# Kernel optimization log

Measured on AMD Instinct MI355X. Metric: run time of the kernel, lower is better.

Reference implementation:

```python
import jax, jax.numpy as jnp
import numpy as np

B, T, C = 4, 2048, 1024
NH = 16
HS = C // NH


def setup_inputs() -> dict:
    key = jax.random.key(0)
    k1, k2, k3, k4, k5 = jax.random.split(key, 5)
    scale = 1.0 / np.sqrt(C)
    return {
        "x": jax.random.normal(k1, (B, T, C), dtype=jnp.float32),
        "Wk": jax.random.normal(k2, (C, C), dtype=jnp.float32) * scale,
        "Wq": jax.random.normal(k3, (C, C), dtype=jnp.float32) * scale,
        "Wv": jax.random.normal(k4, (C, C), dtype=jnp.float32) * scale,
        "Wp": jax.random.normal(k5, (C, C), dtype=jnp.float32) * scale,
    }


def reference(x, Wk, Wq, Wv, Wp):
    b, t, c = x.shape
    # projections (nn.Linear with bias=False computes x @ W.T; weights here are
    # stored so that x @ W is equivalent -- same math, random init either way)
    k = (x @ Wk).reshape(b, t, NH, HS).transpose(0, 2, 1, 3)  # [B,H,T,hs]
    q = (x @ Wq).reshape(b, t, NH, HS).transpose(0, 2, 1, 3)
    v = (x @ Wv).reshape(b, t, NH, HS).transpose(0, 2, 1, 3)
    att = jnp.einsum("bhqd,bhkd->bhqk", q, k) / jnp.sqrt(jnp.float32(HS))
    causal = jnp.tril(jnp.ones((t, t), dtype=bool))
    att = jnp.where(causal[None, None, :, :], att, -jnp.inf)
    att = jax.nn.softmax(att, axis=-1)
    y = jnp.einsum("bhqk,bhkd->bhqd", att, v)  # [B,H,T,hs]
    y = y.transpose(0, 2, 1, 3).reshape(b, t, c)
    return y @ Wp
```

## Files before the change

### kernel.cpp

```cpp
#include <hip/hip_runtime.h>
#include <cstddef>
#include <cstdint>


namespace {

typedef unsigned short u16;
typedef unsigned int u32;
typedef __attribute__((ext_vector_type(8))) short s8v;
typedef __attribute__((ext_vector_type(4))) short s4v;
typedef __attribute__((ext_vector_type(4))) float f4v;

constexpr int Bn = 4, Tn = 2048, Cn = 1024;
constexpr int Mn = Bn * Tn;
constexpr int KVB = 128;
constexpr int NT128 = Tn / 128;
constexpr float QSCALE = 0.125f * 1.44269504f;

__device__ __forceinline__ u16 bfc(float f) {
  return __builtin_bit_cast(u16, (__bf16)f);
}

__device__ __forceinline__ float ex2(float x) {
#if __has_builtin(__builtin_amdgcn_exp2f)
  return __builtin_amdgcn_exp2f(x);
#else
  return exp2f(x);
#endif
}

__device__ __forceinline__ f4v mfma16(s8v a, s8v b, f4v c) {
  return __builtin_amdgcn_mfma_f32_16x16x32_bf16(a, b, c, 0, 0, 0);
}

__device__ __forceinline__ f4v mfma16k16(s4v a, s4v b, f4v c) {
#if __has_builtin(__builtin_amdgcn_mfma_f32_16x16x16bf16_1k)
  return __builtin_amdgcn_mfma_f32_16x16x16bf16_1k(a, b, c, 0, 0, 0);
#else
  f4v d = c;
  asm("v_mfma_f32_16x16x16_bf16 %0, %1, %2, %0" : "+v"(d) : "v"(a), "v"(b));
  return d;
#endif
}

typedef __attribute__((address_space(1))) const u32 gas_u32;
typedef __attribute__((address_space(3))) u32 las_u32;
__device__ __forceinline__ void gl_lds16(const void* g, void* l) {
  __builtin_amdgcn_global_load_lds((gas_u32*)g, (las_u32*)l, 16, 0, 0);
}

__global__ __launch_bounds__(256) void cvtx(const float* __restrict__ in,
                                            u16* __restrict__ out) {
  const size_t i = ((size_t)blockIdx.x * 256 + threadIdx.x) * 8;
  const float4 a = *(const float4*)(in + i);
  const float4 b = *(const float4*)(in + i + 4);
  alignas(16) u16 t[8] = {bfc(a.x), bfc(a.y), bfc(a.z), bfc(a.w),
                          bfc(b.x), bfc(b.y), bfc(b.z), bfc(b.w)};
  *(s8v*)(out + i) = *(const s8v*)t;
}

__global__ __launch_bounds__(256) void wtrans(
    const float* __restrict__ w0, const float* __restrict__ w1,
    const float* __restrict__ w2, const float* __restrict__ w3,
    u16* __restrict__ o0, u16* __restrict__ o1, u16* __restrict__ o2,
    u16* __restrict__ o3) {
  const float* W;
  u16* O;
  switch (blockIdx.z) {
    case 0: W = w0; O = o0; break;
    case 1: W = w1; O = o1; break;
    case 2: W = w2; O = o2; break;
    default: W = w3; O = o3; break;
  }
  __shared__ float Tsh[64][65];
  const int tid = threadIdx.x;
  const int n0 = blockIdx.x * 64, k0 = blockIdx.y * 64;
  {
    const int rk = tid >> 2, c0 = (tid & 3) * 16;
#pragma unroll
    for (int u = 0; u < 4; ++u) {
      const float4 v = *(const float4*)&W[(size_t)(k0 + rk) * Cn + n0 + c0 + u * 4];
      Tsh[rk][c0 + u * 4 + 0] = v.x;
      Tsh[rk][c0 + u * 4 + 1] = v.y;
      Tsh[rk][c0 + u * 4 + 2] = v.z;
      Tsh[rk][c0 + u * 4 + 3] = v.w;
    }
  }
  __syncthreads();
  {
    const int rn = tid >> 2, ck0 = (tid & 3) * 16;
    alignas(16) u16 t[16];
#pragma unroll
    for (int u = 0; u < 16; ++u) t[u] = bfc(Tsh[ck0 + u][rn]);
    *(s8v*)&O[(size_t)(n0 + rn) * Cn + k0 + ck0] = *(const s8v*)&t[0];
    *(s8v*)&O[(size_t)(n0 + rn) * Cn + k0 + ck0 + 8] = *(const s8v*)&t[8];
  }
}

template <int OUT_MODE>
__device__ __forceinline__ void gemm_body(const u16* __restrict__ A,
                                          const u16* __restrict__ Bt,
                                          void* __restrict__ Cout, int bm,
                                          int bn, u16* As, u16* Bs) {
  const int N = Cn, K = Cn;
  const int tid = threadIdx.x;
  const int l = tid & 63, w = tid >> 6;
  const int lr = l & 15, lh = l >> 4;
  const int lrow = tid >> 2;
  const int lkcol = (tid & 3) * 8;
  const u16* Ag = A + (size_t)(bm * 128 + lrow) * K + lkcol;
  const u16* Bg = Bt + (size_t)(bn * 128 + lrow) * K + lkcol;
  const int wm = (w >> 1) * 64, wn = (w & 1) * 64;
  f4v acc[4][4] = {};
  for (int k0 = 0; k0 < K; k0 += 32) {
    __syncthreads();
    gl_lds16(Ag + k0, &As[(size_t)tid * 8]);
    gl_lds16(Ag + (size_t)64 * K + k0, &As[2048 + (size_t)tid * 8]);
    gl_lds16(Bg + k0, &Bs[(size_t)tid * 8]);
    gl_lds16(Bg + (size_t)64 * K + k0, &Bs[2048 + (size_t)tid * 8]);
    __syncthreads();
    s8v af[4], bfr[4];
#pragma unroll
    for (int i = 0; i < 4; ++i)
      af[i] = *(const s8v*)&As[(wm + i * 16 + lr) * 32 + lh * 8];
#pragma unroll
    for (int j = 0; j < 4; ++j)
      bfr[j] = *(const s8v*)&Bs[(wn + j * 16 + lr) * 32 + lh * 8];
    __builtin_amdgcn_s_setprio(1);
#pragma unroll
    for (int i = 0; i < 4; ++i)
#pragma unroll
      for (int j = 0; j < 4; ++j)
        acc[i][j] = mfma16(af[i], bfr[j], acc[i][j]);
    __builtin_amdgcn_s_setprio(0);
  }
  if (OUT_MODE == 2) {
    float* Cf = (float*)Cout;
#pragma unroll
    for (int i = 0; i < 4; ++i) {
      const int row = bm * 128 + wm + i * 16 + lh * 4;
#pragma unroll
      for (int j = 0; j < 4; ++j) {
        const int col = bn * 128 + wn + j * 16 + lr;
#pragma unroll
        for (int r = 0; r < 4; ++r)
          Cf[(size_t)(row + r) * N + col] = acc[i][j][r];
      }
    }
  } else if (OUT_MODE == 0 || OUT_MODE == 3) {
    u16* Cb = (u16*)Cout;
    const float sc = (OUT_MODE == 3) ? QSCALE : 1.0f;
#pragma unroll
    for (int i = 0; i < 4; ++i) {
      const int row = bm * 128 + wm + i * 16 + lh * 4;
#pragma unroll
      for (int j = 0; j < 4; ++j) {
        const int col = bn * 128 + wn + j * 16 + lr;
#pragma unroll
        for (int r = 0; r < 4; ++r)
          Cb[(size_t)(row + r) * N + col] = bfc(acc[i][j][r] * sc);
      }
    }
  } else {
    u16* Vt = (u16*)Cout;
#pragma unroll
    for (int i = 0; i < 4; ++i) {
      const int row0 = bm * 128 + wm + i * 16 + lh * 4;
      const int bq = row0 >> 11;
      const int t0g = row0 & 2047;
      const int tau = t0g & 127;
      const int taup = ((tau >> 5) << 5) | (((tau >> 2) & 3) << 3) |
                       (((tau >> 4) & 1) << 2);
      const int t0p = (t0g & ~127) | taup;
#pragma unroll
      for (int j = 0; j < 4; ++j) {
        const int col = bn * 128 + wn + j * 16 + lr;
        const int hh = col >> 6, dd = col & 63;
        alignas(8) u16 t4[4];
#pragma unroll
        for (int r = 0; r < 4; ++r) t4[r] = bfc(acc[i][j][r]);
        *(s4v*)&Vt[((size_t)((bq * 16 + hh) * 64 + dd)) * Tn + t0p] =
            *(const s4v*)t4;
      }
    }
  }
}

__global__ __launch_bounds__(256) void gemm_qkv(
    const u16* __restrict__ A, const u16* __restrict__ btq,
    const u16* __restrict__ btk, const u16* __restrict__ btv,
    u16* __restrict__ qb, u16* __restrict__ kb, u16* __restrict__ vt) {
  __shared__ __align__(16) u16 As[4096], Bs[4096];
  const int bid = blockIdx.x;
  const int wg = (bid & 7) * 192 + (bid >> 3);
  const int which = wg >> 9, inner = wg & 511;
  const int bm = inner & 63, bn = inner >> 6;
  if (which == 0)
    gemm_body<3>(A, btq, qb, bm, bn, As, Bs);
  else if (which == 1)
    gemm_body<0>(A, btk, kb, bm, bn, As, Bs);
  else
    gemm_body<1>(A, btv, vt, bm, bn, As, Bs);
}

template <int OUT_MODE>
__global__ __launch_bounds__(256) void gemm_bt(const u16* __restrict__ A,
                                               const u16* __restrict__ Bt,
                                               void* __restrict__ Cout) {
  __shared__ __align__(16) u16 As[4096], Bs[4096];
  const int bid = blockIdx.x;
  const int wg = (bid & 7) * 64 + (bid >> 3);
  const int bm = wg & 63, bn = wg >> 6;
  gemm_body<OUT_MODE>(A, Bt, Cout, bm, bn, As, Bs);
}

__device__ __forceinline__ void stage_kv(const u16* __restrict__ kgb,
                                         const u16* __restrict__ vtb,
                                         u16* __restrict__ Kb,
                                         u16* __restrict__ Vb, int k0,
                                         int tid) {
#pragma unroll
  for (int is = 0; is < 2; ++is) {
    const int slot = is * 512 + tid;
    const int row = slot >> 3, ch = slot & 7;
    gl_lds16(kgb + (size_t)(k0 + row) * Cn + ((ch ^ (row & 7)) * 8),
             &Kb[slot * 8]);
  }
#pragma unroll
  for (int is = 0; is < 2; ++is) {
    const int slot = is * 512 + tid;
    const int d = slot >> 4, ch = slot & 15;
    gl_lds16(vtb + (size_t)d * Tn + k0 + ((ch ^ (d & 7)) * 8), &Vb[slot * 8]);
  }
}

__device__ __forceinline__ void attn_step(const s8v (&aq)[2],
                                          const u16* __restrict__ Ks,
                                          const u16* __restrict__ Vs, int kb0,
                                          int kb1, const int (&vch)[4], int ln,
                                          int lh, bool diag, int k0, int qg,
                                          float& m_i, float& l_i, f4v* o) {
  f4v s[8] = {};
  __builtin_amdgcn_s_setprio(1);
#pragma unroll
  for (int n = 0; n < 8; ++n) {
    const s8v bk0 = *(const s8v*)&Ks[kb0 + n * 1024];
    const s8v bk1 = *(const s8v*)&Ks[kb1 + n * 1024];
    s[n] = mfma16(bk0, aq[0], s[n]);
    s[n] = mfma16(bk1, aq[1], s[n]);
  }
  __builtin_amdgcn_s_setprio(0);
  float rm = -1e30f;
  if (diag) {
#pragma unroll
    for (int n = 0; n < 8; ++n)
#pragma unroll
      for (int r = 0; r < 4; ++r) {
        float x = s[n][r];
        if (k0 + n * 16 + lh * 4 + r > qg) x = -1e30f;
        s[n][r] = x;
        rm = fmaxf(rm, x);
      }
  } else {
#pragma unroll
    for (int n = 0; n < 8; ++n)
      rm = fmaxf(rm, fmaxf(fmaxf(s[n][0], s[n][1]), fmaxf(s[n][2], s[n][3])));
  }
  if (!__all(rm <= m_i + 11.5f)) {
    float rr = fmaxf(rm, __shfl_xor(rm, 16));
    rr = fmaxf(rr, __shfl_xor(rr, 32));
    const float mnew = fmaxf(m_i, rr);
    const float al = ex2(m_i - mnew);
    m_i = mnew;
    l_i *= al;
#pragma unroll
    for (int r = 0; r < 4; ++r) {
      const float ar = __shfl(al, (ln & 48) | (lh * 4 + r));
#pragma unroll
      for (int n2 = 0; n2 < 4; ++n2) o[n2][r] *= ar;
    }
  }
  s4v pa[8];
  float rs = 0.f;
#pragma unroll
  for (int n = 0; n < 8; ++n) {
    const float p0 = ex2(s[n][0] - m_i);
    const float p1 = ex2(s[n][1] - m_i);
    const float p2 = ex2(s[n][2] - m_i);
    const float p3 = ex2(s[n][3] - m_i);
    rs += (p0 + p1) + (p2 + p3);
    pa[n] = (s4v){(short)bfc(p0), (short)bfc(p1), (short)bfc(p2),
                  (short)bfc(p3)};
  }
  l_i += rs;
  __builtin_amdgcn_s_setprio(1);
#pragma unroll
  for (int n2 = 0; n2 < 4; ++n2) {
#pragma unroll
    for (int p = 0; p < 4; ++p) {
      const s8v vv = *(const s8v*)&Vs[vch[p] + n2 * 2048];
      const s4v lo = {vv[0], vv[1], vv[2], vv[3]};
      const s4v hi = {vv[4], vv[5], vv[6], vv[7]};
      o[n2] = mfma16k16(pa[2 * p], lo, o[n2]);
      o[n2] = mfma16k16(pa[2 * p + 1], hi, o[n2]);
    }
  }
  __builtin_amdgcn_s_setprio(0);
}

__global__ __launch_bounds__(512) void attn_big(const u16* __restrict__ qg,
                                                const u16* __restrict__ kg,
                                                const u16* __restrict__ vtg,
                                                u16* __restrict__ yg) {
  __shared__ __align__(16) u16 Ks0[KVB * 64], Ks1[KVB * 64];
  __shared__ __align__(16) u16 Vs0[64 * KVB], Vs1[64 * KVB];
  const int tid = threadIdx.x;
  const int ln = tid & 63, w = tid >> 6;
  const int lr = ln & 15, lh = ln >> 4;
  const int bid = blockIdx.x;
  const int wg = (bid & 7) * 64 + (bid >> 3);
  const int bh = wg >> 3, xp = wg & 7;
  const int b = bh >> 4, h = bh & 15;
  const int tL = xp, tH = NT128 - 1 - xp;
  const int q0L = tL * 128, q0H = tH * 128;
  const u16* kgb = kg + (size_t)(b * Tn) * Cn + h * 64;
  const u16* vtb = vtg + (size_t)(bh * 64) * Tn;
  const int kb0 = lr * 64 + ((lh) ^ (lr & 7)) * 8;
  const int kb1 = lr * 64 + ((4 + lh) ^ (lr & 7)) * 8;
  int vch[4];
#pragma unroll
  for (int p = 0; p < 4; ++p)
    vch[p] = lr * 128 + ((p * 4 + lh) ^ (lr & 7)) * 8;
  s8v aqL[2], aqH[2];
  {
    const int row = w * 16 + lr;
#pragma unroll
    for (int kd = 0; kd < 2; ++kd) {
      aqL[kd] = *(const s8v*)&qg[(size_t)(b * Tn + q0L + row) * Cn + h * 64 +
                                 kd * 32 + lh * 8];
      aqH[kd] = *(const s8v*)&qg[(size_t)(b * Tn + q0H + row) * Cn + h * 64 +
                                 kd * 32 + lh * 8];
    }
  }
  const int qgH = q0H + w * 16 + lr;
  const int qgL = q0L + w * 16 + lr;
  float mL = -1e30f, lL = 0.f, mH = -1e30f, lH = 0.f;
  f4v oL[4] = {}, oH[4] = {};
  stage_kv(kgb, vtb, Ks0, Vs0, 0, tid);
  __syncthreads();
  for (int kt = 0; kt <= tH; ++kt) {
    const bool cur = kt & 1;
    const u16* Kb = cur ? Ks1 : Ks0;
    const u16* Vb = cur ? Vs1 : Vs0;
    if (kt < tH)
      stage_kv(kgb, vtb, cur ? Ks0 : Ks1, cur ? Vs0 : Vs1, (kt + 1) * KVB,
               tid);
    attn_step(aqH, Kb, Vb, kb0, kb1, vch, ln, lh, kt == tH, kt * KVB, qgH, mH,
              lH, oH);
    if (kt <= tL)
      attn_step(aqL, Kb, Vb, kb0, kb1, vch, ln, lh, kt == tL, kt * KVB, qgL,
                mL, lL, oL);
    __syncthreads();
  }
  {
    float ls = lH;
    ls += __shfl_xor(ls, 16);
    ls += __shfl_xor(ls, 32);
    const float linv = 1.0f / ls;
#pragma unroll
    for (int r = 0; r < 4; ++r) {
      const float iv = __shfl(linv, (ln & 48) | (lh * 4 + r));
      const int row = q0H + w * 16 + lh * 4 + r;
#pragma unroll
      for (int n2 = 0; n2 < 4; ++n2)
        yg[(size_t)(b * Tn + row) * Cn + h * 64 + n2 * 16 + lr] =
            bfc(oH[n2][r] * iv);
    }
  }
  {
    float ls = lL;
    ls += __shfl_xor(ls, 16);
    ls += __shfl_xor(ls, 32);
    const float linv = 1.0f / ls;
#pragma unroll
    for (int r = 0; r < 4; ++r) {
      const float iv = __shfl(linv, (ln & 48) | (lh * 4 + r));
      const int row = q0L + w * 16 + lh * 4 + r;
#pragma unroll
      for (int n2 = 0; n2 < 4; ++n2)
        yg[(size_t)(b * Tn + row) * Cn + h * 64 + n2 * 16 + lr] =
            bfc(oL[n2][r] * iv);
    }
  }
}

}

extern "C" void kernel_launch(void* const* d_in, const int* in_sizes, int n_in,
                              void* d_out, int out_size, void* d_ws,
                              size_t ws_size, hipStream_t stream) {
  (void)in_sizes; (void)n_in; (void)out_size; (void)ws_size;
  const float* x = (const float*)d_in[0];
  const float* Wk = (const float*)d_in[1];
  const float* Wq = (const float*)d_in[2];
  const float* Wv = (const float*)d_in[3];
  const float* Wp = (const float*)d_in[4];
  float* out = (float*)d_out;
  char* ws = (char*)d_ws;

  u16* xb = (u16*)(ws);
  u16* wqt = (u16*)(ws + 16777216);
  u16* wkt = (u16*)(ws + 18874368);
  u16* wvt = (u16*)(ws + 20971520);
  u16* wpt = (u16*)(ws + 23068672);
  u16* qb = (u16*)(ws + 25165824);
  u16* kb = (u16*)(ws + 41943040);
  u16* vt = (u16*)(ws + 58720256);
  u16* yb = (u16*)(ws + 75497472);

  cvtx<<<dim3(4096), dim3(256), 0, stream>>>(x, xb);
  wtrans<<<dim3(16, 16, 4), dim3(256), 0, stream>>>(Wq, Wk, Wv, Wp, wqt, wkt,
                                                    wvt, wpt);
  gemm_qkv<<<dim3(1536), dim3(256), 0, stream>>>(xb, wqt, wkt, wvt, qb, kb,
                                                 vt);
  attn_big<<<dim3(512), dim3(512), 0, stream>>>(qb, kb, vt, yb);
  gemm_bt<2><<<dim3(512), dim3(256), 0, stream>>>(yb, wpt, out);
}
```

Measured before the change: 186.6 us.

## Merge prep kernels, deepen GEMM K-tile with XOR-swizzled LDS, remap blocks per XCD

Folds the x-to-bf16 conversion and the weight transpose into a single prep launch, removing one kernel launch. The GEMM K step grows from 32 to 64, which halves the barrier pairs per tile at the cost of double the LDS per block. An XOR swizzle on the LDS columns is meant to avoid bank conflicts on the 128-byte rows. Block-to-tile mapping is changed so each XCD handles a contiguous band of M rows, aiming for better L2 reuse of A.

```diff
diff --git a/kernel.cpp b/kernel.cpp
--- a/kernel.cpp
+++ b/kernel.cpp
@@ -49,32 +49,35 @@
   __builtin_amdgcn_global_load_lds((gas_u32*)g, (las_u32*)l, 16, 0, 0);
 }
 
-__global__ __launch_bounds__(256) void cvtx(const float* __restrict__ in,
-                                            u16* __restrict__ out) {
-  const size_t i = ((size_t)blockIdx.x * 256 + threadIdx.x) * 8;
-  const float4 a = *(const float4*)(in + i);
-  const float4 b = *(const float4*)(in + i + 4);
-  alignas(16) u16 t[8] = {bfc(a.x), bfc(a.y), bfc(a.z), bfc(a.w),
-                          bfc(b.x), bfc(b.y), bfc(b.z), bfc(b.w)};
-  *(s8v*)(out + i) = *(const s8v*)t;
-}
-
-__global__ __launch_bounds__(256) void wtrans(
+__global__ __launch_bounds__(256) void prep(
+    const float* __restrict__ x, u16* __restrict__ xb,
     const float* __restrict__ w0, const float* __restrict__ w1,
     const float* __restrict__ w2, const float* __restrict__ w3,
     u16* __restrict__ o0, u16* __restrict__ o1, u16* __restrict__ o2,
     u16* __restrict__ o3) {
+  __shared__ float Tsh[64][65];
+  const int bid = blockIdx.x;
+  const int tid = threadIdx.x;
+  if (bid < 4096) {
+    const size_t i = ((size_t)bid * 256 + tid) * 8;
+    const float4 a = *(const float4*)(x + i);
+    const float4 b = *(const float4*)(x + i + 4);
+    alignas(16) u16 t[8] = {bfc(a.x), bfc(a.y), bfc(a.z), bfc(a.w),
+                            bfc(b.x), bfc(b.y), bfc(b.z), bfc(b.w)};
+    *(s8v*)(xb + i) = *(const s8v*)t;
+    return;
+  }
+  const int idx = bid - 4096;
+  const int wz = idx >> 8, wy = (idx >> 4) & 15, wx = idx & 15;
   const float* W;
   u16* O;
-  switch (blockIdx.z) {
+  switch (wz) {
     case 0: W = w0; O = o0; break;
     case 1: W = w1; O = o1; break;
     case 2: W = w2; O = o2; break;
     default: W = w3; O = o3; break;
   }
-  __shared__ float Tsh[64][65];
-  const int tid = threadIdx.x;
-  const int n0 = blockIdx.x * 64, k0 = blockIdx.y * 64;
+  const int n0 = wx * 64, k0 = wy * 64;
   {
     const int rk = tid >> 2, c0 = (tid & 3) * 16;
 #pragma unroll
@@ -106,33 +109,45 @@
   const int tid = threadIdx.x;
   const int l = tid & 63, w = tid >> 6;
   const int lr = l & 15, lh = l >> 4;
-  const int lrow = tid >> 2;
-  const int lkcol = (tid & 3) * 8;
-  const u16* Ag = A + (size_t)(bm * 128 + lrow) * K + lkcol;
-  const u16* Bg = Bt + (size_t)(bn * 128 + lrow) * K + lkcol;
   const int wm = (w >> 1) * 64, wn = (w & 1) * 64;
+  const u16* Ab = A + (size_t)(bm * 128) * K;
+  const u16* Bb = Bt + (size_t)(bn * 128) * K;
+  const int sw = lr & 7;
   f4v acc[4][4] = {};
-  for (int k0 = 0; k0 < K; k0 += 32) {
+  for (int k0 = 0; k0 < K; k0 += 64) {
     __syncthreads();
-    gl_lds16(Ag + k0, &As[(size_t)tid * 8]);
-    gl_lds16(Ag + (size_t)64 * K + k0, &As[2048 + (size_t)tid * 8]);
-    gl_lds16(Bg + k0, &Bs[(size_t)tid * 8]);
-    gl_lds16(Bg + (size_t)64 * K + k0, &Bs[2048 + (size_t)tid * 8]);
+#pragma unroll
+    for (int i = 0; i < 4; ++i) {
+      const int s = tid + 256 * i;
+      const int r = s >> 3, c = s & 7;
+      gl_lds16(Ab + (size_t)r * K + k0 + ((c ^ (r & 7)) * 8), &As[s * 8]);
+    }
+#pragma unroll
+    for (int i = 0; i < 4; ++i) {
+      const int s = tid + 256 * i;
+      const int r = s >> 3, c = s & 7;
+      gl_lds16(Bb + (size_t)r * K + k0 + ((c ^ (r & 7)) * 8), &Bs[s * 8]);
+    }
     __syncthreads();
-    s8v af[4], bfr[4];
-#pragma unroll
-    for (int i = 0; i < 4; ++i)
-      af[i] = *(const s8v*)&As[(wm + i * 16 + lr) * 32 + lh * 8];
-#pragma unroll
-    for (int j = 0; j < 4; ++j)
-      bfr[j] = *(const s8v*)&Bs[(wn + j * 16 + lr) * 32 + lh * 8];
-    __builtin_amdgcn_s_setprio(1);
-#pragma unroll
-    for (int i = 0; i < 4; ++i)
+#pragma unroll
+    for (int half = 0; half < 2; ++half) {
+      s8v af[4], bfr[4];
+#pragma unroll
+      for (int i = 0; i < 4; ++i)
+        af[i] = *(const s8v*)&As[(wm + i * 16 + lr) * 64 +
+                                 (((half * 4 + lh) ^ sw) * 8)];
 #pragma unroll
       for (int j = 0; j < 4; ++j)
-        acc[i][j] = mfma16(af[i], bfr[j], acc[i][j]);
-    __builtin_amdgcn_s_setprio(0);
+        bfr[j] = *(const s8v*)&Bs[(wn + j * 16 + lr) * 64 +
+                                  (((half * 4 + lh) ^ sw) * 8)];
+      __builtin_amdgcn_s_setprio(1);
+#pragma unroll
+      for (int i = 0; i < 4; ++i)
+#pragma unroll
+        for (int j = 0; j < 4; ++j)
+          acc[i][j] = mfma16(af[i], bfr[j], acc[i][j]);
+      __builtin_amdgcn_s_setprio(0);
+    }
   }
   if (OUT_MODE == 2) {
     float* Cf = (float*)Cout;
@@ -190,11 +205,12 @@
     const u16* __restrict__ A, const u16* __restrict__ btq,
     const u16* __restrict__ btk, const u16* __restrict__ btv,
     u16* __restrict__ qb, u16* __restrict__ kb, u16* __restrict__ vt) {
-  __shared__ __align__(16) u16 As[4096], Bs[4096];
+  __shared__ __align__(16) u16 As[8192], Bs[8192];
   const int bid = blockIdx.x;
-  const int wg = (bid & 7) * 192 + (bid >> 3);
-  const int which = wg >> 9, inner = wg & 511;
-  const int bm = inner & 63, bn = inner >> 6;
+  const int xcd = bid & 7, j = bid >> 3;
+  const int bm = xcd * 8 + (j & 7);
+  const int combo = j >> 3;
+  const int which = combo >> 3, bn = combo & 7;
   if (which == 0)
     gemm_body<3>(A, btq, qb, bm, bn, As, Bs);
   else if (which == 1)
@@ -207,10 +223,11 @@
 __global__ __launch_bounds__(256) void gemm_bt(const u16* __restrict__ A,
                                                const u16* __restrict__ Bt,
                                                void* __restrict__ Cout) {
-  __shared__ __align__(16) u16 As[4096], Bs[4096];
+  __shared__ __align__(16) u16 As[8192], Bs[8192];
   const int bid = blockIdx.x;
-  const int wg = (bid & 7) * 64 + (bid >> 3);
-  const int bm = wg & 63, bn = wg >> 6;
+  const int xcd = bid & 7, j = bid >> 3;
+  const int bm = xcd * 8 + (j & 7);
+  const int bn = j >> 3;
   gemm_body<OUT_MODE>(A, Bt, Cout, bm, bn, As, Bs);
 }
 
@@ -418,9 +435,8 @@
   u16* vt = (u16*)(ws + 58720256);
   u16* yb = (u16*)(ws + 75497472);
 
-  cvtx<<<dim3(4096), dim3(256), 0, stream>>>(x, xb);
-  wtrans<<<dim3(16, 16, 4), dim3(256), 0, stream>>>(Wq, Wk, Wv, Wp, wqt, wkt,
-                                                    wvt, wpt);
+  prep<<<dim3(5120), dim3(256), 0, stream>>>(x, xb, Wq, Wk, Wv, Wp, wqt, wkt,
+                                             wvt, wpt);
   gemm_qkv<<<dim3(1536), dim3(256), 0, stream>>>(xb, wqt, wkt, wvt, qb, kb,
                                                  vt);
   attn_big<<<dim3(512), dim3(512), 0, stream>>>(qb, kb, vt, yb);
```

After: 169.0 us. 9.4% less time.
